# Performance work log

Measured on AMD Instinct MI355X. Metric: run time of the kernel, lower is better.

The kernel has to match this reference:

```python
import jax, jax.numpy as jnp
import numpy as np

B, GL, GF, N = 4, 4, 128, 1024
CS, CN, NA = 32, 16, 16
S, HS = 512, 512


def squash(s, axis):
    # mag_sq/(1+mag_sq) * s/mag == s * mag/(1+mag_sq)
    mag_sq = jnp.sum(s * s, axis=axis, keepdims=True)
    return s * (jnp.sqrt(mag_sq) / (1.0 + mag_sq))


def routing(u_hat, n_iter=3):
    # u_hat: [M, I, J, U]; dynamic routing, softmax over J, squash over J (as in source)
    M, I, J, U = u_hat.shape
    b = jnp.zeros((I, J), dtype=u_hat.dtype)
    v = None
    for _ in range(n_iter):
        c = jax.nn.softmax(b, axis=1)                       # [I, J]
        s = jnp.einsum('ij,miju->mju', c, u_hat)            # [M, J, U]
        v = squash(s, axis=1)                               # squash over J (torch dim=2)
        b = b + jnp.einsum('miju,mju->mij', u_hat, v).mean(axis=0)
    return v


def setup_inputs():
    key = jax.random.key(0)
    ks = jax.random.split(key, 7)
    sc = 0.1
    return {
        'graph_embed': jax.random.normal(ks[0], (B, GL, GF, N), jnp.float32),
        'hidden': jax.random.normal(ks[1], (B, S, HS), jnp.float32),
        'Wp': jax.random.normal(ks[2], (GL, CS, GL, GF), jnp.float32) * sc,  # per-unit conv kernels
        'bp': jax.random.normal(ks[3], (GL, CS), jnp.float32) * sc,
        'Wg': jax.random.normal(ks[4], (CS, CN, CS, GL), jnp.float32) * sc,  # graph caps [I,J,U,K]
        'Wa': jax.random.normal(ks[5], (CS + HS,), jnp.float32) * sc,        # attention_1 weight
        'Ws': jax.random.normal(ks[6], (CN, NA, CS, CS), jnp.float32) * sc,  # aspect caps [I,J,U,K]
    }


def _per_example(x, h, Wp, bp, Wg, Wa, Ws):
    # x: [GL, GF, N], h: [S, HS]
    gl, gf, n = x.shape
    # primary capsules: each unit's conv kernel covers all (GL,GF) -> full contraction
    u = jnp.einsum('uclf,lfn->ucn', Wp, x) + bp[:, :, None]   # [GL, CS, N]
    u = squash(u.reshape(gl, -1), axis=1)                     # squash over CS*N (torch dim=2)
    p = u.reshape(n, gl, CS)                                  # torch .view(-1, GL, CS)
    # graph capsule routing
    u_hat_g = jnp.einsum('ijuk,mik->miju', Wg, p.transpose(0, 2, 1))  # [N, CS, CN, CS]
    v_g = routing(u_hat_g)                                    # [N, CN, CS]
    g = v_g.reshape(n, CS, CN).mean(axis=0).reshape(CN, CS)   # torch .view semantics
    # adaptive attention: Linear([g;h]) with no bias, softmax over capsules
    score = jax.nn.softmax((g @ Wa[:CS])[None, :] + (h @ Wa[CS:])[:, None], axis=1)  # [S, CN]
    condensed = g[None, :, :] * score[:, :, None]             # [S, CN, CS]
    # aspect capsule routing (transpose(1,2) then layer-internal transpose cancel out)
    u_hat_a = jnp.einsum('ijuk,mik->miju', Ws, condensed)     # [S, CN, NA, CS]
    return routing(u_hat_a)                                   # [S, NA, CS]


def reference(graph_embed, hidden, Wp, bp, Wg, Wa, Ws):
    f = jax.vmap(_per_example, in_axes=(0, 0, None, None, None, None, None))
    return f(graph_embed, hidden, Wp, bp, Wg, Wa, Ws)   # [B, S, NA, CS]
```

## Files before the change

### kernel.cpp

```cpp
#include <hip/hip_runtime.h>
#include <math.h>


static constexpr int OFF_U   = 0;
static constexpr int OFF_S   = 524288;
static constexpr int OFF_SS  = 2621440;
static constexpr int OFF_BG  = 2621456;
static constexpr int OFF_G   = 2623504;
static constexpr int OFF_VA  = 2625552;
static constexpr int OFF_MS  = 2627600;
static constexpr int OFF_UH  = 2758672;
static constexpr int OFF_WGR = 2791440;

__global__ void k_primary_part(const float* __restrict__ X, const float* __restrict__ Wp,
                               float* __restrict__ Upart,
                               const float* __restrict__ Wg, float* __restrict__ Wgr)
{
    __shared__ float Wt[128 * 68];
    const int t = threadIdx.x;
    if (blockIdx.z == 16) {
        const int blk = blockIdx.x * 16 + blockIdx.y;
#pragma unroll
        for (int r = 0; r < 8; ++r) {
            const int e = blk * 2048 + r * 256 + t;
            const int q = e >> 9, rem = e & 511;
            const int u = rem >> 4, j = rem & 15;
            const int i = q & 31, kk = q >> 5;
            Wgr[e] = Wg[((i * 16 + j) * 32 + u) * 4 + kk];
        }
        return;
    }
    const int ct = blockIdx.x, nt = blockIdx.y;
    const int b = blockIdx.z >> 2, ks = blockIdx.z & 3;
    const int tn = t & 15, tc = t >> 4;
    const int c0 = ct * 64, n0 = nt * 64;
#pragma unroll
    for (int i = 0; i < 8; ++i) {
        const int idx = t + i * 256;
        const int c = idx >> 5, k4 = idx & 31;
        const float4 wv = *(const float4*)&Wp[(size_t)(c0 + c) * 512 + ks * 128 + k4 * 4];
        Wt[(k4 * 4 + 0) * 68 + c] = wv.x;
        Wt[(k4 * 4 + 1) * 68 + c] = wv.y;
        Wt[(k4 * 4 + 2) * 68 + c] = wv.z;
        Wt[(k4 * 4 + 3) * 68 + c] = wv.w;
    }
    __syncthreads();
    float acc[4][4] = {};
    const float* Xp = X + (size_t)b * 524288 + (size_t)(ks * 128) * 1024 + n0 + tn * 4;
#pragma unroll 4
    for (int k = 0; k < 128; ++k) {
        const float4 xv = *(const float4*)(Xp + (size_t)k * 1024);
        const float4 wv = *(const float4*)&Wt[k * 68 + tc * 4];
        const float w[4] = {wv.x, wv.y, wv.z, wv.w};
        const float x[4] = {xv.x, xv.y, xv.z, xv.w};
#pragma unroll
        for (int ci = 0; ci < 4; ++ci)
#pragma unroll
            for (int ni = 0; ni < 4; ++ni)
                acc[ci][ni] = fmaf(w[ci], x[ni], acc[ci][ni]);
    }
    float* up = Upart + (size_t)ks * 524288 + (size_t)b * 131072;
#pragma unroll
    for (int ci = 0; ci < 4; ++ci)
        *(float4*)&up[(size_t)(c0 + tc * 4 + ci) * 1024 + n0 + tn * 4] =
            make_float4(acc[ci][0], acc[ci][1], acc[ci][2], acc[ci][3]);
}

__global__ void k_reduceU(const float* __restrict__ Upart, const float* __restrict__ bp,
                          float* __restrict__ U, float* __restrict__ SS)
{
    __shared__ float red[256];
    const int blk = blockIdx.x, t = threadIdx.x;
    const int b = blk >> 5, cg = blk & 31;
    float ssq = 0.f;
#pragma unroll
    for (int i = 0; i < 4; ++i) {
        const int c = cg * 4 + i;
        const int f4 = b * 32768 + c * 256 + t;
        float4 s = ((const float4*)Upart)[f4];
#pragma unroll
        for (int ks = 1; ks < 4; ++ks) {
            const float4 p = ((const float4*)Upart)[ks * 131072 + f4];
            s.x += p.x; s.y += p.y; s.z += p.z; s.w += p.w;
        }
        const float bv = bp[c];
        s.x += bv; s.y += bv; s.z += bv; s.w += bv;
        ssq = fmaf(s.x, s.x, ssq); ssq = fmaf(s.y, s.y, ssq);
        ssq = fmaf(s.z, s.z, ssq); ssq = fmaf(s.w, s.w, ssq);
        ((float4*)U)[f4] = s;
    }
    red[t] = ssq;
    __syncthreads();
    for (int s = 128; s > 0; s >>= 1) {
        if (t < s) red[t] += red[t + s];
        __syncthreads();
    }
    if (t == 0) atomicAdd(&SS[b * 4 + (cg >> 3)], red[0]);
}

__global__ __launch_bounds__(256) void k_smatmulM(
    const float* __restrict__ U, const float* __restrict__ SS,
    const float* __restrict__ Bg, const float* __restrict__ Wgr,
    float* __restrict__ S, float* __restrict__ MS, float* __restrict__ G)
{
    __shared__ __align__(16) float Pt[64 * 68];
    __shared__ __align__(16) float Ct[64 * 160];
    __shared__ float cls[512];
    __shared__ float gacc[128];
    const int mt = blockIdx.x, us = blockIdx.y, b = blockIdx.z;
    const int t = threadIdx.x;
    const int tm = t >> 4;
    const int uu = t & 7, jh = (t >> 3) & 1;
    const int m0 = mt * 64;

    if (t < 32) {
        float vals[16];
        float mx = -1e30f;
        for (int j = 0; j < 16; ++j) { vals[j] = Bg[b * 512 + t * 16 + j]; mx = fmaxf(mx, vals[j]); }
        float sum = 0.f;
        for (int j = 0; j < 16; ++j) { vals[j] = expf(vals[j] - mx); sum += vals[j]; }
        const float inv = 1.f / sum;
        for (int j = 0; j < 16; ++j) cls[t * 16 + j] = vals[j] * inv;
    }
    if (G != nullptr && t < 128) gacc[t] = 0.f;
    const float ss = SS[b * 4 + (mt >> 2)];
    const float sc = sqrtf(ss) / (1.f + ss);
    float acc[4][8] = {};
    const float* Ub = U + (size_t)b * 131072 + (size_t)m0 * 128;
    __syncthreads();

    for (int kc = 0; kc < 2; ++kc) {
#pragma unroll
        for (int it = 0; it < 4; ++it) {
            const int x = t + it * 256;
            const int m = x & 63, q4 = x >> 6;
            const float4 v = *(const float4*)&Ub[(size_t)m * 128 + kc * 64 + q4 * 4];
            Pt[(q4 * 4 + 0) * 68 + m] = v.x * sc;
            Pt[(q4 * 4 + 1) * 68 + m] = v.y * sc;
            Pt[(q4 * 4 + 2) * 68 + m] = v.z * sc;
            Pt[(q4 * 4 + 3) * 68 + m] = v.w * sc;
        }
#pragma unroll
        for (int it = 0; it < 8; ++it) {
            const int x = t + it * 256;
            const int c4 = (x & 31) * 4, qL = x >> 5;
            const int q = kc * 64 + qL;
            const int i = q & 31;
            const int j0 = c4 & 15;
            const float4 w = *(const float4*)&Wgr[(size_t)q * 512 + us * 128 + c4];
            const int cp = qL * 160 + c4 + ((c4 >> 4) << 2);
            Ct[cp + 0] = cls[i * 16 + j0 + 0] * w.x;
            Ct[cp + 1] = cls[i * 16 + j0 + 1] * w.y;
            Ct[cp + 2] = cls[i * 16 + j0 + 2] * w.z;
            Ct[cp + 3] = cls[i * 16 + j0 + 3] * w.w;
        }
        __syncthreads();
        const int cbase = uu * 20 + jh * 8;
#pragma unroll 4
        for (int qL = 0; qL < 64; ++qL) {
            const float4 p4 = *(const float4*)&Pt[qL * 68 + tm * 4];
            const float4 ca = *(const float4*)&Ct[qL * 160 + cbase];
            const float4 cb = *(const float4*)&Ct[qL * 160 + cbase + 4];
            const float pm[4] = {p4.x, p4.y, p4.z, p4.w};
            const float cj[8] = {ca.x, ca.y, ca.z, ca.w, cb.x, cb.y, cb.z, cb.w};
#pragma unroll
            for (int mm = 0; mm < 4; ++mm)
#pragma unroll
                for (int jj = 0; jj < 8; ++jj)
                    acc[mm][jj] = fmaf(pm[mm], cj[jj], acc[mm][jj]);
        }
        __syncthreads();
    }

#pragma unroll
    for (int mm = 0; mm < 4; ++mm) {
        float* Sp = S + (size_t)b * 524288 + (size_t)(m0 + tm * 4 + mm) * 512 + us * 8 + uu;
#pragma unroll
        for (int jj = 0; jj < 8; ++jj)
            Sp[(jh * 8 + jj) * 32] = acc[mm][jj];
    }

    if (G == nullptr) {
#pragma unroll
        for (int mm = 0; mm < 4; ++mm) {
            float msq = 0.f;
#pragma unroll
            for (int jj = 0; jj < 8; ++jj) msq = fmaf(acc[mm][jj], acc[mm][jj], msq);
            msq += __shfl_xor(msq, 8);
            if (jh == 0)
                MS[b * 32768 + (m0 + tm * 4 + mm) * 32 + us * 8 + uu] =
                    sqrtf(msq) / (1.f + msq);
        }
    } else {
        float part[8];
#pragma unroll
        for (int jj = 0; jj < 8; ++jj) part[jj] = 0.f;
#pragma unroll
        for (int mm = 0; mm < 4; ++mm) {
            float msq = 0.f;
#pragma unroll
            for (int jj = 0; jj < 8; ++jj) msq = fmaf(acc[mm][jj], acc[mm][jj], msq);
            msq += __shfl_xor(msq, 8);
            const float msc = sqrtf(msq) / (1.f + msq);
#pragma unroll
            for (int jj = 0; jj < 8; ++jj) part[jj] = fmaf(acc[mm][jj], msc, part[jj]);
        }
#pragma unroll
        for (int jj = 0; jj < 8; ++jj)
            atomicAdd(&gacc[(jh * 8 + jj) * 8 + uu], part[jj]);
        __syncthreads();
        if (t < 128) {
            const int j = t >> 3, u2 = t & 7;
            atomicAdd(&G[b * 512 + j * 32 + us * 8 + u2], gacc[t] * (1.f / 1024.f));
        }
    }
}

__global__ void k_tbu(const float* __restrict__ U, const float* __restrict__ SS,
                      const float* __restrict__ S, const float* __restrict__ MS,
                      const float* __restrict__ Wg, float* __restrict__ Bg)
{
    __shared__ float Ps[64 * 132];
    __shared__ float Vs[64 * 68];
    __shared__ float bup[64];
    const int jt = blockIdx.x, mc = blockIdx.y, b = blockIdx.z;
    const int t = threadIdx.x;
    const int tq = t & 31, tjv = t >> 5;
    const int m0 = mc * 64;
    if (t < 64) bup[t] = 0.f;
    const float ss = SS[b * 4 + (mc >> 2)];
    const float sc = sqrtf(ss) / (1.f + ss);
#pragma unroll
    for (int i = 0; i < 8; ++i) {
        const int f4 = t + i * 256;
        const int r = f4 >> 5, q4 = f4 & 31;
        float4 v = *(const float4*)&U[(size_t)b * 131072 + (size_t)(m0 + r) * 128 + q4 * 4];
        v.x *= sc; v.y *= sc; v.z *= sc; v.w *= sc;
        *(float4*)&Ps[r * 132 + q4 * 4] = v;
    }
#pragma unroll
    for (int i = 0; i < 4; ++i) {
        const int f4 = t + i * 256;
        const int r = f4 >> 4, c4 = f4 & 15;
        const int m = m0 + r;
        float4 v = *(const float4*)&S[(size_t)b * 524288 + (size_t)m * 512 + jt * 64 + c4 * 4];
        const int ub = (c4 * 4) & 31;
        const float* msp = MS + b * 32768 + m * 32;
        v.x *= msp[ub + 0]; v.y *= msp[ub + 1]; v.z *= msp[ub + 2]; v.w *= msp[ub + 3];
        *(float4*)&Vs[r * 68 + c4 * 4] = v;
    }
    __syncthreads();
    float acc[4][8] = {};
#pragma unroll 2
    for (int m = 0; m < 64; ++m) {
        const float4 p4 = *(const float4*)&Ps[m * 132 + tq * 4];
        const float4 va = *(const float4*)&Vs[m * 68 + tjv * 8];
        const float4 vb = *(const float4*)&Vs[m * 68 + tjv * 8 + 4];
        const float pv[4] = {p4.x, p4.y, p4.z, p4.w};
        const float vv[8] = {va.x, va.y, va.z, va.w, vb.x, vb.y, vb.z, vb.w};
#pragma unroll
        for (int qi = 0; qi < 4; ++qi)
#pragma unroll
            for (int ji = 0; ji < 8; ++ji)
                acc[qi][ji] = fmaf(pv[qi], vv[ji], acc[qi][ji]);
    }
    const int k = tq >> 3;
    const int j_loc = tjv >> 2;
    const int j = jt * 2 + j_loc;
    const int u0 = (tjv & 3) * 8;
#pragma unroll
    for (int qi = 0; qi < 4; ++qi) {
        const int i = (tq & 7) * 4 + qi;
        const float* wp = Wg + ((i * 16 + j) * 32) * 4 + k;
        float s = 0.f;
#pragma unroll
        for (int ji = 0; ji < 8; ++ji)
            s = fmaf(wp[(u0 + ji) * 4], acc[qi][ji], s);
        s += __shfl_xor(s, 8);
        s += __shfl_xor(s, 16);
        s += __shfl_xor(s, 32);
        if ((t & 56) == 0) atomicAdd(&bup[i * 2 + j_loc], s);
    }
    __syncthreads();
    if (t < 64) {
        const int ii = t >> 1, jl = t & 1;
        atomicAdd(&Bg[b * 512 + ii * 16 + jt * 2 + jl], bup[t] * (1.f / 1024.f));
    }
}

__global__ void k_uhat(const float* __restrict__ G, const float* __restrict__ Wa,
                       const float* __restrict__ Ws, float* __restrict__ UH)
{
    const int b = blockIdx.y;
    const int t = threadIdx.x;
    __shared__ float g[512], cond[512], score[16], red[16];
    g[t] = G[b * 512 + t];
    g[t + 256] = G[b * 512 + 256 + t];
    __syncthreads();
    if (t < 16) {
        float s = 0.f;
        for (int u = 0; u < 32; ++u) s = fmaf(g[t * 32 + u], Wa[u], s);
        red[t] = s;
    }
    __syncthreads();
    if (t == 0) {
        float mx = -1e30f;
        for (int j = 0; j < 16; ++j) mx = fmaxf(mx, red[j]);
        float sum = 0.f;
        for (int j = 0; j < 16; ++j) { score[j] = expf(red[j] - mx); sum += score[j]; }
        const float inv = 1.f / sum;
        for (int j = 0; j < 16; ++j) score[j] *= inv;
    }
    __syncthreads();
    cond[t] = g[t] * score[t >> 5];
    cond[t + 256] = g[t + 256] * score[(t + 256) >> 5];
    __syncthreads();
    const int e0 = blockIdx.x * 1024 + t * 4;
    const int i = e0 >> 9;
    const float* cp = cond + i * 32;
    const float* wp = Ws + (size_t)e0 * 32;
    float res[4];
#pragma unroll
    for (int jj = 0; jj < 4; ++jj) {
        float s = 0.f;
#pragma unroll
        for (int k8 = 0; k8 < 8; ++k8) {
            const float4 w = *(const float4*)(wp + jj * 32 + k8 * 4);
            s = fmaf(w.x, cp[k8 * 4 + 0], s);
            s = fmaf(w.y, cp[k8 * 4 + 1], s);
            s = fmaf(w.z, cp[k8 * 4 + 2], s);
            s = fmaf(w.w, cp[k8 * 4 + 3], s);
        }
        res[jj] = s;
    }
    ((float4*)UH)[(b * 8192 + e0) >> 2] = make_float4(res[0], res[1], res[2], res[3]);
}

__global__ void k_route(const float* __restrict__ UH, float* __restrict__ VA)
{
    const int b = blockIdx.x;
    const int t = threadIdx.x;
    __shared__ float uh[8192], ba[256], cc[256], sbuf[512], msc[32];
#pragma unroll
    for (int i = 0; i < 8; ++i)
        ((float4*)uh)[i * 256 + t] = ((const float4*)UH)[b * 2048 + i * 256 + t];
    ba[t] = 0.f;
    __syncthreads();
    for (int it = 0; it < 3; ++it) {
        if (t < 16) {
            float mx = -1e30f;
            for (int j = 0; j < 16; ++j) mx = fmaxf(mx, ba[t * 16 + j]);
            float sum = 0.f;
            for (int j = 0; j < 16; ++j) { cc[t * 16 + j] = expf(ba[t * 16 + j] - mx); sum += cc[t * 16 + j]; }
            const float inv = 1.f / sum;
            for (int j = 0; j < 16; ++j) cc[t * 16 + j] *= inv;
        }
        __syncthreads();
        for (int h = 0; h < 2; ++h) {
            const int e = h * 256 + t;
            const int j = e >> 5;
            float s = 0.f;
            for (int i = 0; i < 16; ++i) s = fmaf(cc[i * 16 + j], uh[i * 512 + e], s);
            sbuf[e] = s;
        }
        __syncthreads();
        if (t < 32) {
            float mg = 0.f;
            for (int j = 0; j < 16; ++j) { const float x = sbuf[j * 32 + t]; mg = fmaf(x, x, mg); }
            msc[t] = sqrtf(mg) / (1.f + mg);
        }
        __syncthreads();
        for (int h = 0; h < 2; ++h) {
            const int e = h * 256 + t;
            sbuf[e] *= msc[e & 31];
        }
        __syncthreads();
        if (it < 2) {
            const int i = t >> 4, j = t & 15;
            float s = 0.f;
            for (int u = 0; u < 32; ++u) s = fmaf(uh[i * 512 + j * 32 + u], sbuf[j * 32 + u], s);
            ba[t] += s;
            __syncthreads();
        }
    }
    VA[b * 512 + t] = sbuf[t];
    VA[b * 512 + 256 + t] = sbuf[256 + t];
}

__global__ void k_out(const float* __restrict__ VA, float* __restrict__ out)
{
    const int idx = blockIdx.x * 256 + threadIdx.x;
    const int b = idx >> 16;
    const int jv4 = idx & 127;
    ((float4*)out)[idx] = ((const float4*)VA)[b * 128 + jv4];
}

extern "C" void kernel_launch(void* const* d_in, const int* in_sizes, int n_in,
                              void* d_out, int out_size, void* d_ws, size_t ws_size,
                              hipStream_t stream)
{
    const float* X   = (const float*)d_in[0];
    const float* Wp  = (const float*)d_in[2];
    const float* bp  = (const float*)d_in[3];
    const float* Wg  = (const float*)d_in[4];
    const float* Wa  = (const float*)d_in[5];
    const float* Wsp = (const float*)d_in[6];
    float* out = (float*)d_out;
    float* ws = (float*)d_ws;

    float* U   = ws + OFF_U;
    float* S   = ws + OFF_S;
    float* SS  = ws + OFF_SS;
    float* Bg  = ws + OFF_BG;
    float* G   = ws + OFF_G;
    float* VA  = ws + OFF_VA;
    float* MS  = ws + OFF_MS;
    float* UH  = ws + OFF_UH;
    float* Wgr = ws + OFF_WGR;

    hipMemsetAsync(SS, 0, (16 + 2048 + 2048) * sizeof(float), stream);

    k_primary_part<<<dim3(2, 16, 17), 256, 0, stream>>>(X, Wp, S, Wg, Wgr);
    k_reduceU<<<128, 256, 0, stream>>>(S, bp, U, SS);

    k_smatmulM<<<dim3(16, 4, 4), 256, 0, stream>>>(U, SS, Bg, Wgr, S, MS, nullptr);
    k_tbu<<<dim3(8, 16, 4), 256, 0, stream>>>(U, SS, S, MS, Wg, Bg);
    k_smatmulM<<<dim3(16, 4, 4), 256, 0, stream>>>(U, SS, Bg, Wgr, S, MS, nullptr);
    k_tbu<<<dim3(8, 16, 4), 256, 0, stream>>>(U, SS, S, MS, Wg, Bg);
    k_smatmulM<<<dim3(16, 4, 4), 256, 0, stream>>>(U, SS, Bg, Wgr, S, nullptr, G);

    k_uhat<<<dim3(8, 4), 256, 0, stream>>>(G, Wa, Wsp, UH);
    k_route<<<4, 256, 0, stream>>>(UH, VA);
    k_out<<<1024, 256, 0, stream>>>(VA, out);
}
```

Before: 196.4 us.

## Fuse split-K primary reduction and replace global atomics with deterministic partial buffers

Folds the split-K partial-sum reduction and bias/sum-of-squares step into the primary GEMM kernel, so each block loops over all four K chunks and writes U directly with per-block sum-of-squares partials. Global atomicAdds for the routing logits and graph capsule mean become per-block partial slots that consumers reduce on load, and the initial memset plus the reduceU launch are removed. The first routing iteration uses a constant uniform softmax instead of reading zeroed logits. The cost is four times fewer blocks in the primary GEMM (128 instead of 512), which lowers parallelism, plus extra partial-sum reads in each consumer.

```diff
diff --git a/kernel.cpp b/kernel.cpp
--- a/kernel.cpp
+++ b/kernel.cpp
@@ -4,21 +4,23 @@
 
 static constexpr int OFF_U   = 0;
 static constexpr int OFF_S   = 524288;
-static constexpr int OFF_SS  = 2621440;
-static constexpr int OFF_BG  = 2621456;
-static constexpr int OFF_G   = 2623504;
-static constexpr int OFF_VA  = 2625552;
-static constexpr int OFF_MS  = 2627600;
-static constexpr int OFF_UH  = 2758672;
-static constexpr int OFF_WGR = 2791440;
-
-__global__ void k_primary_part(const float* __restrict__ X, const float* __restrict__ Wp,
-                               float* __restrict__ Upart,
-                               const float* __restrict__ Wg, float* __restrict__ Wgr)
+static constexpr int OFF_SSP = 2621440;
+static constexpr int OFF_BGP = 2621696;
+static constexpr int OFF_GP  = 2654464;
+static constexpr int OFF_VA  = 2687232;
+static constexpr int OFF_MS  = 2689280;
+static constexpr int OFF_UH  = 2820352;
+static constexpr int OFF_WGR = 2853120;
+
+__global__ void k_primaryF(const float* __restrict__ X, const float* __restrict__ Wp,
+                           const float* __restrict__ bp,
+                           float* __restrict__ U, float* __restrict__ SSp,
+                           const float* __restrict__ Wg, float* __restrict__ Wgr)
 {
     __shared__ float Wt[128 * 68];
+    __shared__ float red[256];
     const int t = threadIdx.x;
-    if (blockIdx.z == 16) {
+    if (blockIdx.z == 4) {
         const int blk = blockIdx.x * 16 + blockIdx.y;
 #pragma unroll
         for (int r = 0; r < 8; ++r) {
@@ -30,82 +32,68 @@
         }
         return;
     }
-    const int ct = blockIdx.x, nt = blockIdx.y;
-    const int b = blockIdx.z >> 2, ks = blockIdx.z & 3;
+    const int ct = blockIdx.x, nt = blockIdx.y, b = blockIdx.z;
     const int tn = t & 15, tc = t >> 4;
     const int c0 = ct * 64, n0 = nt * 64;
-#pragma unroll
-    for (int i = 0; i < 8; ++i) {
-        const int idx = t + i * 256;
-        const int c = idx >> 5, k4 = idx & 31;
-        const float4 wv = *(const float4*)&Wp[(size_t)(c0 + c) * 512 + ks * 128 + k4 * 4];
-        Wt[(k4 * 4 + 0) * 68 + c] = wv.x;
-        Wt[(k4 * 4 + 1) * 68 + c] = wv.y;
-        Wt[(k4 * 4 + 2) * 68 + c] = wv.z;
-        Wt[(k4 * 4 + 3) * 68 + c] = wv.w;
-    }
-    __syncthreads();
     float acc[4][4] = {};
-    const float* Xp = X + (size_t)b * 524288 + (size_t)(ks * 128) * 1024 + n0 + tn * 4;
+    for (int ks = 0; ks < 4; ++ks) {
+        if (ks) __syncthreads();
+#pragma unroll
+        for (int i = 0; i < 8; ++i) {
+            const int idx = t + i * 256;
+            const int c = idx >> 5, k4 = idx & 31;
+            const float4 wv = *(const float4*)&Wp[(size_t)(c0 + c) * 512 + ks * 128 + k4 * 4];
+            Wt[(k4 * 4 + 0) * 68 + c] = wv.x;
+            Wt[(k4 * 4 + 1) * 68 + c] = wv.y;
+            Wt[(k4 * 4 + 2) * 68 + c] = wv.z;
+            Wt[(k4 * 4 + 3) * 68 + c] = wv.w;
+        }
+        __syncthreads();
+        const float* Xp = X + (size_t)b * 524288 + (size_t)(ks * 128) * 1024 + n0 + tn * 4;
 #pragma unroll 4
-    for (int k = 0; k < 128; ++k) {
-        const float4 xv = *(const float4*)(Xp + (size_t)k * 1024);
-        const float4 wv = *(const float4*)&Wt[k * 68 + tc * 4];
-        const float w[4] = {wv.x, wv.y, wv.z, wv.w};
-        const float x[4] = {xv.x, xv.y, xv.z, xv.w};
-#pragma unroll
-        for (int ci = 0; ci < 4; ++ci)
-#pragma unroll
-            for (int ni = 0; ni < 4; ++ni)
-                acc[ci][ni] = fmaf(w[ci], x[ni], acc[ci][ni]);
-    }
-    float* up = Upart + (size_t)ks * 524288 + (size_t)b * 131072;
-#pragma unroll
-    for (int ci = 0; ci < 4; ++ci)
-        *(float4*)&up[(size_t)(c0 + tc * 4 + ci) * 1024 + n0 + tn * 4] =
-            make_float4(acc[ci][0], acc[ci][1], acc[ci][2], acc[ci][3]);
-}
-
-__global__ void k_reduceU(const float* __restrict__ Upart, const float* __restrict__ bp,
-                          float* __restrict__ U, float* __restrict__ SS)
-{
-    __shared__ float red[256];
-    const int blk = blockIdx.x, t = threadIdx.x;
-    const int b = blk >> 5, cg = blk & 31;
+        for (int k = 0; k < 128; ++k) {
+            const float4 xv = *(const float4*)(Xp + (size_t)k * 1024);
+            const float4 wv = *(const float4*)&Wt[k * 68 + tc * 4];
+            const float w[4] = {wv.x, wv.y, wv.z, wv.w};
+            const float x[4] = {xv.x, xv.y, xv.z, xv.w};
+#pragma unroll
+            for (int ci = 0; ci < 4; ++ci)
+#pragma unroll
+                for (int ni = 0; ni < 4; ++ni)
+                    acc[ci][ni] = fmaf(w[ci], x[ni], acc[ci][ni]);
+        }
+    }
     float ssq = 0.f;
 #pragma unroll
-    for (int i = 0; i < 4; ++i) {
-        const int c = cg * 4 + i;
-        const int f4 = b * 32768 + c * 256 + t;
-        float4 s = ((const float4*)Upart)[f4];
-#pragma unroll
-        for (int ks = 1; ks < 4; ++ks) {
-            const float4 p = ((const float4*)Upart)[ks * 131072 + f4];
-            s.x += p.x; s.y += p.y; s.z += p.z; s.w += p.w;
-        }
+    for (int ci = 0; ci < 4; ++ci) {
+        const int c = c0 + tc * 4 + ci;
         const float bv = bp[c];
-        s.x += bv; s.y += bv; s.z += bv; s.w += bv;
-        ssq = fmaf(s.x, s.x, ssq); ssq = fmaf(s.y, s.y, ssq);
-        ssq = fmaf(s.z, s.z, ssq); ssq = fmaf(s.w, s.w, ssq);
-        ((float4*)U)[f4] = s;
+        float4 o = make_float4(acc[ci][0] + bv, acc[ci][1] + bv,
+                               acc[ci][2] + bv, acc[ci][3] + bv);
+        ssq = fmaf(o.x, o.x, ssq); ssq = fmaf(o.y, o.y, ssq);
+        ssq = fmaf(o.z, o.z, ssq); ssq = fmaf(o.w, o.w, ssq);
+        *(float4*)&U[(size_t)b * 131072 + (size_t)c * 1024 + n0 + tn * 4] = o;
     }
     red[t] = ssq;
     __syncthreads();
-    for (int s = 128; s > 0; s >>= 1) {
-        if (t < s) red[t] += red[t + s];
-        __syncthreads();
-    }
-    if (t == 0) atomicAdd(&SS[b * 4 + (cg >> 3)], red[0]);
-}
-
-__global__ __launch_bounds__(256) void k_smatmulM(
-    const float* __restrict__ U, const float* __restrict__ SS,
-    const float* __restrict__ Bg, const float* __restrict__ Wgr,
-    float* __restrict__ S, float* __restrict__ MS, float* __restrict__ G)
+    for (int s = 64; s > 0; s >>= 1) {
+        if ((t & 127) < s) red[t] += red[t + s];
+        __syncthreads();
+    }
+    if ((t & 127) == 0)
+        SSp[(b * 4 + ct * 2 + (t >> 7)) * 16 + nt] = red[t];
+}
+
+__global__ __launch_bounds__(256) void k_smatmulM2(
+    const float* __restrict__ U, const float* __restrict__ SSp,
+    const float* __restrict__ Bgp, const float* __restrict__ Wgr,
+    float* __restrict__ S, float* __restrict__ MS, float* __restrict__ Gp,
+    const int bg0)
 {
     __shared__ __align__(16) float Pt[64 * 68];
     __shared__ __align__(16) float Ct[64 * 160];
     __shared__ float cls[512];
+    __shared__ float bgs[512];
     __shared__ float gacc[128];
     const int mt = blockIdx.x, us = blockIdx.y, b = blockIdx.z;
     const int t = threadIdx.x;
@@ -113,18 +101,36 @@
     const int uu = t & 7, jh = (t >> 3) & 1;
     const int m0 = mt * 64;
 
-    if (t < 32) {
-        float vals[16];
-        float mx = -1e30f;
-        for (int j = 0; j < 16; ++j) { vals[j] = Bg[b * 512 + t * 16 + j]; mx = fmaxf(mx, vals[j]); }
-        float sum = 0.f;
-        for (int j = 0; j < 16; ++j) { vals[j] = expf(vals[j] - mx); sum += vals[j]; }
-        const float inv = 1.f / sum;
-        for (int j = 0; j < 16; ++j) cls[t * 16 + j] = vals[j] * inv;
-    }
-    if (G != nullptr && t < 128) gacc[t] = 0.f;
-    const float ss = SS[b * 4 + (mt >> 2)];
-    const float sc = sqrtf(ss) / (1.f + ss);
+    if (bg0) {
+        cls[t] = 0.0625f;
+        cls[t + 256] = 0.0625f;
+    } else {
+#pragma unroll
+        for (int h = 0; h < 2; ++h) {
+            const int p = t + h * 256;
+            const int i = p >> 4, j = p & 15;
+            float s = 0.f;
+#pragma unroll 4
+            for (int mc = 0; mc < 16; ++mc)
+                s += Bgp[((b * 16 + mc) * 8 + (j >> 1)) * 64 + i * 2 + (j & 1)];
+            bgs[p] = s * (1.f / 1024.f);
+        }
+        __syncthreads();
+        if (t < 32) {
+            float vals[16];
+            float mx = -1e30f;
+            for (int j = 0; j < 16; ++j) { vals[j] = bgs[t * 16 + j]; mx = fmaxf(mx, vals[j]); }
+            float sum = 0.f;
+            for (int j = 0; j < 16; ++j) { vals[j] = expf(vals[j] - mx); sum += vals[j]; }
+            const float inv = 1.f / sum;
+            for (int j = 0; j < 16; ++j) cls[t * 16 + j] = vals[j] * inv;
+        }
+    }
+    if (Gp != nullptr && t < 128) gacc[t] = 0.f;
+    float ssum = 0.f;
+#pragma unroll
+    for (int i = 0; i < 16; ++i) ssum += SSp[(b * 4 + (mt >> 2)) * 16 + i];
+    const float sc = sqrtf(ssum) / (1.f + ssum);
     float acc[4][8] = {};
     const float* Ub = U + (size_t)b * 131072 + (size_t)m0 * 128;
     __syncthreads();
@@ -180,7 +186,7 @@
             Sp[(jh * 8 + jj) * 32] = acc[mm][jj];
     }
 
-    if (G == nullptr) {
+    if (Gp == nullptr) {
 #pragma unroll
         for (int mm = 0; mm < 4; ++mm) {
             float msq = 0.f;
@@ -211,14 +217,16 @@
         __syncthreads();
         if (t < 128) {
             const int j = t >> 3, u2 = t & 7;
-            atomicAdd(&G[b * 512 + j * 32 + us * 8 + u2], gacc[t] * (1.f / 1024.f));
-        }
-    }
-}
-
-__global__ void k_tbu(const float* __restrict__ U, const float* __restrict__ SS,
-                      const float* __restrict__ S, const float* __restrict__ MS,
-                      const float* __restrict__ Wg, float* __restrict__ Bg)
+            Gp[(size_t)(b * 16 + mt) * 512 + j * 32 + us * 8 + u2] =
+                gacc[t] * (1.f / 1024.f);
+        }
+    }
+}
+
+__global__ void k_tbu2(const float* __restrict__ U, const float* __restrict__ SSp,
+                       const float* __restrict__ S, const float* __restrict__ MS,
+                       const float* __restrict__ Wg, float* __restrict__ Bgp,
+                       const int first)
 {
     __shared__ float Ps[64 * 132];
     __shared__ float Vs[64 * 68];
@@ -228,8 +236,10 @@
     const int tq = t & 31, tjv = t >> 5;
     const int m0 = mc * 64;
     if (t < 64) bup[t] = 0.f;
-    const float ss = SS[b * 4 + (mc >> 2)];
-    const float sc = sqrtf(ss) / (1.f + ss);
+    float ssum = 0.f;
+#pragma unroll
+    for (int i = 0; i < 16; ++i) ssum += SSp[(b * 4 + (mc >> 2)) * 16 + i];
+    const float sc = sqrtf(ssum) / (1.f + ssum);
 #pragma unroll
     for (int i = 0; i < 8; ++i) {
         const int f4 = t + i * 256;
@@ -283,19 +293,27 @@
     }
     __syncthreads();
     if (t < 64) {
-        const int ii = t >> 1, jl = t & 1;
-        atomicAdd(&Bg[b * 512 + ii * 16 + jt * 2 + jl], bup[t] * (1.f / 1024.f));
-    }
-}
-
-__global__ void k_uhat(const float* __restrict__ G, const float* __restrict__ Wa,
-                       const float* __restrict__ Ws, float* __restrict__ UH)
+        float* slot = &Bgp[((b * 16 + mc) * 8 + jt) * 64 + t];
+        if (first) *slot = bup[t];
+        else       *slot += bup[t];
+    }
+}
+
+__global__ void k_uhat2(const float* __restrict__ Gp, const float* __restrict__ Wa,
+                        const float* __restrict__ Ws, float* __restrict__ UH)
 {
     const int b = blockIdx.y;
     const int t = threadIdx.x;
     __shared__ float g[512], cond[512], score[16], red[16];
-    g[t] = G[b * 512 + t];
-    g[t + 256] = G[b * 512 + 256 + t];
+    float g0 = 0.f, g1 = 0.f;
+#pragma unroll 4
+    for (int mt = 0; mt < 16; ++mt) {
+        const float* gp = Gp + (size_t)(b * 16 + mt) * 512;
+        g0 += gp[t];
+        g1 += gp[t + 256];
+    }
+    g[t] = g0;
+    g[t + 256] = g1;
     __syncthreads();
     if (t < 16) {
         float s = 0.f;
@@ -410,26 +428,24 @@
 
     float* U   = ws + OFF_U;
     float* S   = ws + OFF_S;
-    float* SS  = ws + OFF_SS;
-    float* Bg  = ws + OFF_BG;
-    float* G   = ws + OFF_G;
+    float* SSp = ws + OFF_SSP;
+    float* Bgp = ws + OFF_BGP;
+    float* Gp  = ws + OFF_GP;
     float* VA  = ws + OFF_VA;
     float* MS  = ws + OFF_MS;
     float* UH  = ws + OFF_UH;
     float* Wgr = ws + OFF_WGR;
 
-    hipMemsetAsync(SS, 0, (16 + 2048 + 2048) * sizeof(float), stream);
-
-    k_primary_part<<<dim3(2, 16, 17), 256, 0, stream>>>(X, Wp, S, Wg, Wgr);
-    k_reduceU<<<128, 256, 0, stream>>>(S, bp, U, SS);
-
-    k_smatmulM<<<dim3(16, 4, 4), 256, 0, stream>>>(U, SS, Bg, Wgr, S, MS, nullptr);
-    k_tbu<<<dim3(8, 16, 4), 256, 0, stream>>>(U, SS, S, MS, Wg, Bg);
-    k_smatmulM<<<dim3(16, 4, 4), 256, 0, stream>>>(U, SS, Bg, Wgr, S, MS, nullptr);
-    k_tbu<<<dim3(8, 16, 4), 256, 0, stream>>>(U, SS, S, MS, Wg, Bg);
-    k_smatmulM<<<dim3(16, 4, 4), 256, 0, stream>>>(U, SS, Bg, Wgr, S, nullptr, G);
-
-    k_uhat<<<dim3(8, 4), 256, 0, stream>>>(G, Wa, Wsp, UH);
+
+    k_primaryF<<<dim3(2, 16, 5), 256, 0, stream>>>(X, Wp, bp, U, SSp, Wg, Wgr);
+
+    k_smatmulM2<<<dim3(16, 4, 4), 256, 0, stream>>>(U, SSp, Bgp, Wgr, S, MS, nullptr, 1);
+    k_tbu2<<<dim3(8, 16, 4), 256, 0, stream>>>(U, SSp, S, MS, Wg, Bgp, 1);
+    k_smatmulM2<<<dim3(16, 4, 4), 256, 0, stream>>>(U, SSp, Bgp, Wgr, S, MS, nullptr, 0);
+    k_tbu2<<<dim3(8, 16, 4), 256, 0, stream>>>(U, SSp, S, MS, Wg, Bgp, 0);
+    k_smatmulM2<<<dim3(16, 4, 4), 256, 0, stream>>>(U, SSp, Bgp, Wgr, S, nullptr, Gp, 0);
+
+    k_uhat2<<<dim3(8, 4), 256, 0, stream>>>(Gp, Wa, Wsp, UH);
     k_route<<<4, 256, 0, stream>>>(UH, VA);
     k_out<<<1024, 256, 0, stream>>>(VA, out);
 }
```

New measurement: 230.6 us. +17.4%, slower.
